# Kernel tuning notes

Measured on AMD Instinct MI355X. Metric: run time of the kernel, lower is better.

The kernel has to match this reference:

```python
import jax, jax.numpy as jnp
import numpy as np

N, E, R, G = 50000, 800000, 8, 128
IN_EMBD, LAYER, OUT = 64, 256, 256
CARDS = [33, 5, 3, 4, 2, 3]
EPS = 1e-5


def setup_inputs() -> dict:
    key = jax.random.key(0)
    ks = iter(jax.random.split(key, 40))
    d = {}
    # int inputs
    cols = [jax.random.randint(next(ks), (N,), 0, c) for c in CARDS]
    d['x'] = jnp.stack(cols, axis=1)                                  # [N,6]
    d['edge_index'] = jax.random.randint(next(ks), (2, E), 0, N)      # [2,E]
    d['edge_type'] = jax.random.randint(next(ks), (E,), 0, R)         # [E]
    d['batch'] = jnp.sort(jax.random.randint(next(ks), (N,), 0, G))   # [N]
    # embedding tables
    for i, c in enumerate(CARDS):
        d[f'emb{i}'] = jax.random.normal(next(ks), (c, IN_EMBD), jnp.float32)
    # RGCNConv1
    d['W1'] = jax.random.normal(next(ks), (R, 6 * IN_EMBD, LAYER), jnp.float32) * 0.05
    d['root1'] = jax.random.normal(next(ks), (6 * IN_EMBD, LAYER), jnp.float32) * 0.05
    d['b1'] = jnp.zeros((LAYER,), jnp.float32)
    # RGCNConv2
    d['W2'] = jax.random.normal(next(ks), (R, LAYER, OUT), jnp.float32) * 0.05
    d['root2'] = jax.random.normal(next(ks), (LAYER, OUT), jnp.float32) * 0.05
    d['b2'] = jnp.zeros((OUT,), jnp.float32)
    # gate_nn: Linear -> BatchNorm1d -> ReLU -> Linear(.,1)
    d['Wg1'] = jax.random.normal(next(ks), (OUT, OUT), jnp.float32) * 0.05
    d['bg1'] = jnp.zeros((OUT,), jnp.float32)
    d['gamma'] = jnp.ones((OUT,), jnp.float32)
    d['beta'] = jnp.zeros((OUT,), jnp.float32)
    d['Wg2'] = jax.random.normal(next(ks), (OUT, 1), jnp.float32) * 0.05
    d['bg2'] = jnp.zeros((1,), jnp.float32)
    # graph head
    d['Wgl'] = jax.random.normal(next(ks), (OUT, 1), jnp.float32) * 0.05
    d['bgl'] = jnp.zeros((1,), jnp.float32)
    return d


def rgcn_conv(h, src, dst, etype, W, root, b):
    # per-relation transform of all nodes, then gather per edge (avoids per-edge weight gather)
    hr = jnp.einsum('ni,rio->rno', h, W)            # [R,N,out]
    msg = hr[etype, src]                             # [E,out]
    # mean aggregation per (dst, relation), matching PyG RGCNConv default aggr='mean'
    counts = jnp.zeros((h.shape[0], W.shape[0]), h.dtype).at[dst, etype].add(1.0)
    norm = 1.0 / jnp.clip(counts, 1.0)               # [N,R]
    agg = jax.ops.segment_sum(msg * norm[dst, etype][:, None], dst, num_segments=h.shape[0])
    return agg + h @ root + b


def global_attention(x, batch, Wg1, bg1, gamma, beta, Wg2, bg2):
    h = x @ Wg1 + bg1
    mu = jnp.mean(h, axis=0)
    var = jnp.var(h, axis=0)
    h = (h - mu) * jax.lax.rsqrt(var + EPS) * gamma + beta   # BatchNorm1d (batch stats)
    gate = jax.nn.relu(h) @ Wg2 + bg2                        # [N,1]
    gmax = jax.ops.segment_max(gate, batch, num_segments=G)
    e = jnp.exp(gate - gmax[batch])
    denom = jax.ops.segment_sum(e, batch, num_segments=G)
    alpha = e / denom[batch]
    return jax.ops.segment_sum(alpha * x, batch, num_segments=G)  # [G,out]


def reference(x, edge_index, edge_type, batch,
              emb0, emb1, emb2, emb3, emb4, emb5,
              W1, root1, b1, W2, root2, b2,
              Wg1, bg1, gamma, beta, Wg2, bg2, Wgl, bgl):
    tables = [emb0, emb1, emb2, emb3, emb4, emb5]
    h = jnp.concatenate([tables[i][x[:, i]] for i in range(6)], axis=1)  # [N, 6*in_embd]
    src, dst = edge_index[0], edge_index[1]
    h = jax.nn.sigmoid(rgcn_conv(h, src, dst, edge_type, W1, root1, b1))
    h = jax.nn.sigmoid(rgcn_conv(h, src, dst, edge_type, W2, root2, b2))
    pooled = global_attention(h, batch, Wg1, bg1, gamma, beta, Wg2, bg2)
    return jax.nn.sigmoid(pooled @ Wgl + bgl)  # [G,1]
```

## Files before the change

kernel.cpp:

```cpp
#include <hip/hip_runtime.h>
#include <hip/hip_bf16.h>
#include <cstdint>

#define NN 50000
#define EE 800000
#define RR 8
#define GG 128
#define D0 384
#define DL 256
#define NCR 50

typedef __attribute__((ext_vector_type(8))) short bf16x8;
typedef __attribute__((ext_vector_type(4))) float f32x4;

__device__ __forceinline__ float sigmoidf_(float x) { return 1.0f / (1.0f + expf(-x)); }

__device__ __forceinline__ ushort f2bf(float f) {
    uint u = __float_as_uint(f);
    u += 0x7fffu + ((u >> 16) & 1u);
    return (ushort)(u >> 16);
}
__device__ __forceinline__ uint pack2bf(float lo, float hi) {
    return (uint)f2bf(lo) | ((uint)f2bf(hi) << 16);
}
__device__ __forceinline__ float bf2f(ushort u) {
    return __uint_as_float((uint)u << 16);
}

__device__ __forceinline__ void accw8(float* s, uint4 a, float w) {
    s[0] += w * __uint_as_float(a.x << 16);
    s[1] += w * __uint_as_float(a.x & 0xffff0000u);
    s[2] += w * __uint_as_float(a.y << 16);
    s[3] += w * __uint_as_float(a.y & 0xffff0000u);
    s[4] += w * __uint_as_float(a.z << 16);
    s[5] += w * __uint_as_float(a.z & 0xffff0000u);
    s[6] += w * __uint_as_float(a.w << 16);
    s[7] += w * __uint_as_float(a.w & 0xffff0000u);
}

__device__ __forceinline__ void unp8(float* f, uint4 a) {
    f[0] = __uint_as_float(a.x << 16);
    f[1] = __uint_as_float(a.x & 0xffff0000u);
    f[2] = __uint_as_float(a.y << 16);
    f[3] = __uint_as_float(a.y & 0xffff0000u);
    f[4] = __uint_as_float(a.z << 16);
    f[5] = __uint_as_float(a.z & 0xffff0000u);
    f[6] = __uint_as_float(a.w << 16);
    f[7] = __uint_as_float(a.w & 0xffff0000u);
}
__device__ __forceinline__ uint4 pack8bf(const float* f) {
    uint4 p;
    p.x = pack2bf(f[0], f[1]);
    p.y = pack2bf(f[2], f[3]);
    p.z = pack2bf(f[4], f[5]);
    p.w = pack2bf(f[6], f[7]);
    return p;
}

__device__ __forceinline__ unsigned fenc(float x) {
    unsigned u = __float_as_uint(x);
    return (u & 0x80000000u) ? ~u : (u | 0x80000000u);
}
__device__ __forceinline__ float fdec(unsigned u) {
    unsigned b = (u & 0x80000000u) ? (u & 0x7fffffffu) : ~u;
    return __uint_as_float(b);
}

__global__ __launch_bounds__(256) void lutbuild_kernel(
    const float* __restrict__ e0, const float* __restrict__ e1,
    const float* __restrict__ e2, const float* __restrict__ e3,
    const float* __restrict__ e4, const float* __restrict__ e5,
    const float* __restrict__ W1, const float* __restrict__ root1,
    ushort* __restrict__ T)
{
    int b = blockIdx.x;
    int cr = b / 9;
    int r  = b - cr * 9;
    int t, c;
    if      (cr < 33) { t = 0; c = cr; }
    else if (cr < 38) { t = 1; c = cr - 33; }
    else if (cr < 41) { t = 2; c = cr - 38; }
    else if (cr < 45) { t = 3; c = cr - 41; }
    else if (cr < 47) { t = 4; c = cr - 45; }
    else              { t = 5; c = cr - 47; }
    const float* emb;
    switch (t) {
        case 0: emb = e0; break; case 1: emb = e1; break; case 2: emb = e2; break;
        case 3: emb = e3; break; case 4: emb = e4; break; default: emb = e5; break;
    }
    const float* er = emb + c * 64;
    int col = threadIdx.x;
    const float* Wb = (r < 8) ? (W1 + ((size_t)r * D0 + t * 64) * DL + col)
                              : (root1 + (size_t)(t * 64) * DL + col);
    float s = 0.f;
    #pragma unroll 8
    for (int k = 0; k < 64; k++) s += er[k] * Wb[(size_t)k * DL];
    T[(size_t)(cr * 9 + r) * DL + col] = f2bf(s);
}

__global__ __launch_bounds__(256) void lutsum_kernel(
    const ushort* __restrict__ T,
    const int* __restrict__ x,
    ushort* __restrict__ hrc,
    int c0, int chc)
{
    __shared__ ushort Ts[NCR * 256];
    const int rr = blockIdx.y;
    int t = threadIdx.x;
    for (int i = t; i < NCR * 256; i += 256) {
        int cr = i >> 8, col = i & 255;
        Ts[i] = T[(size_t)(cr * 9 + c0 + rr) * 256 + col];
    }
    __syncthreads();

    const int slot = t >> 5;
    const int l    = t & 31;
    const int c    = l * 8;
    const int colbase = rr * 256 + c;

    for (int base = blockIdx.x * 8; base < NN; base += gridDim.x * 8) {
        int n = base + slot;
        if (n < NN) {
            const int* xp = x + n * 6;
            const int cumc[6] = {0, 33, 38, 41, 45, 47};
            float acc[8];
            #pragma unroll
            for (int q = 0; q < 8; q++) acc[q] = 0.f;
            #pragma unroll
            for (int tb = 0; tb < 6; tb++) {
                int cr = cumc[tb] + xp[tb];
                uint4 v = *(const uint4*)&Ts[cr * 256 + c];
                accw8(acc, v, 1.0f);
            }
            *(uint4*)&hrc[(size_t)n * chc + colbase] = pack8bf(acc);
        }
    }
}

__global__ __launch_bounds__(256) void lutfin_kernel(
    const ushort* __restrict__ T, const int* __restrict__ x,
    const ushort* __restrict__ hacc, const float* __restrict__ b1,
    ushort* __restrict__ h1)
{
    __shared__ ushort Ts[NCR * 256];
    int t = threadIdx.x;
    for (int i = t; i < NCR * 256; i += 256) {
        int cr = i >> 8, col = i & 255;
        Ts[i] = T[(size_t)(cr * 9 + 8) * 256 + col];
    }
    __syncthreads();

    const int slot = t >> 5;
    const int l = t & 31;
    const int c = l * 8;

    for (int base = blockIdx.x * 8; base < NN; base += gridDim.x * 8) {
        int n = base + slot;
        if (n < NN) {
            const int* xp = x + n * 6;
            const int cumc[6] = {0, 33, 38, 41, 45, 47};
            float acc[8];
            float4 b0 = *(const float4*)&b1[c];
            float4 bb = *(const float4*)&b1[c + 4];
            acc[0] = b0.x; acc[1] = b0.y; acc[2] = b0.z; acc[3] = b0.w;
            acc[4] = bb.x; acc[5] = bb.y; acc[6] = bb.z; acc[7] = bb.w;
            #pragma unroll
            for (int tb = 0; tb < 6; tb++) {
                int cr = cumc[tb] + xp[tb];
                uint4 v = *(const uint4*)&Ts[cr * 256 + c];
                accw8(acc, v, 1.0f);
            }
            uint4 hv = *(const uint4*)&hacc[(size_t)n * DL + c];
            float hf[8]; unp8(hf, hv);
            #pragma unroll
            for (int q = 0; q < 8; q++) acc[q] = sigmoidf_(acc[q] + hf[q]);
            *(uint4*)&h1[(size_t)n * DL + c] = pack8bf(acc);
        }
    }
}

__global__ __launch_bounds__(256) void cvtT_kernel(
    const float* __restrict__ W, const float* __restrict__ root,
    ushort* __restrict__ WbT, int nrel, int IN)
{
    int idx = blockIdx.x * 256 + threadIdx.x;
    int tot = (nrel + 1) * DL * IN;
    if (idx >= tot) return;
    int k = idx % IN;
    int rn = idx / IN;
    int n = rn % DL;
    int r = rn / DL;
    float v = (r < nrel) ? W[((size_t)r * IN + k) * DL + n] : root[(size_t)k * DL + n];
    WbT[idx] = f2bf(v);
}

__global__ __launch_bounds__(256) void count_kernel(
    const int* __restrict__ dst, const int* __restrict__ et, int* __restrict__ counts)
{
    int i = blockIdx.x * 256 + threadIdx.x;
    if (i < EE) atomicAdd(&counts[dst[i] * RR + et[i]], 1);
}

#define SCAN_CHUNK 4096
__global__ __launch_bounds__(256) void scanA_kernel(const int* __restrict__ cnt, int M, int* __restrict__ blkSums)
{
    __shared__ int s[256];
    int b = blockIdx.x, t = threadIdx.x;
    int base = b * SCAN_CHUNK + t * 16;
    int tot = 0;
    #pragma unroll
    for (int i = 0; i < 16; i++) { int idx = base + i; if (idx < M) tot += cnt[idx]; }
    s[t] = tot; __syncthreads();
    for (int off = 128; off > 0; off >>= 1) {
        if (t < off) s[t] += s[t + off];
        __syncthreads();
    }
    if (t == 0) blkSums[b] = s[0];
}

__global__ void scanB_kernel(const int* __restrict__ blkSums, int NB, int* __restrict__ blkOff)
{
    int l = threadIdx.x;
    int a = (l < NB) ? blkSums[l] : 0;
    int b = (64 + l < NB) ? blkSums[64 + l] : 0;
    int ia = a, ib = b;
    for (int o = 1; o < 64; o <<= 1) {
        int t0 = __shfl_up(ia, o, 64);
        if (l >= o) ia += t0;
        int t1 = __shfl_up(ib, o, 64);
        if (l >= o) ib += t1;
    }
    int tot0 = __shfl(ia, 63, 64);
    if (l < NB) blkOff[l] = ia - a;
    if (64 + l < NB) blkOff[64 + l] = tot0 + ib - b;
}

__global__ __launch_bounds__(256) void scanC_kernel(
    const int* __restrict__ cnt, int M, const int* __restrict__ blkOff,
    int* __restrict__ offs, int* __restrict__ curs)
{
    __shared__ int s[256];
    int b = blockIdx.x, t = threadIdx.x;
    int base = b * SCAN_CHUNK + t * 16;
    int loc[16];
    int tot = 0;
    #pragma unroll
    for (int i = 0; i < 16; i++) {
        int idx = base + i;
        int v = (idx < M) ? cnt[idx] : 0;
        loc[i] = tot; tot += v;
    }
    s[t] = tot; __syncthreads();
    for (int off = 1; off < 256; off <<= 1) {
        int v = (t >= off) ? s[t - off] : 0;
        __syncthreads();
        s[t] += v;
        __syncthreads();
    }
    int texc = s[t] - tot;
    int bb = blkOff[b];
    #pragma unroll
    for (int i = 0; i < 16; i++) {
        int idx = base + i;
        if (idx < M) { int o = bb + texc + loc[i]; offs[idx] = o; curs[idx] = o; }
    }
}

__global__ __launch_bounds__(256) void scatter_kernel(
    const int* __restrict__ src, const int* __restrict__ dst, const int* __restrict__ et,
    const int* __restrict__ cnts, int* __restrict__ cursors,
    int2* __restrict__ epk, int chc, int mask)
{
    int i = blockIdx.x * 256 + threadIdx.x;
    if (i < EE) {
        int r = et[i];
        int b = dst[i] * RR + r;
        int pos = atomicAdd(&cursors[b], 1);
        int2 p;
        p.x = src[i] * chc + (r & mask) * DL;
        p.y = __float_as_int(1.0f / (float)cnts[b]);
        epk[pos] = p;
    }
}

template<int K, int MODE>
__global__ __launch_bounds__(256) void dense_gemm(
    const ushort* __restrict__ A,
    const ushort* __restrict__ Bt,
    const float* __restrict__ bias,
    const ushort* __restrict__ haccp,
    ushort* __restrict__ C,
    int M, int NCOL)
{
    constexpr int NKT = K / 64;
    __shared__ __attribute__((aligned(16))) ushort Al[2][128 * 64];
    __shared__ __attribute__((aligned(16))) ushort Bl[2][128 * 64];

    const int nwg  = gridDim.x * gridDim.y;
    const int flat = blockIdx.y * gridDim.x + blockIdx.x;
    const int q8 = nwg >> 3, r8 = nwg & 7;
    const int xcd = flat & 7, pos = flat >> 3;
    const int vid = ((xcd < r8) ? xcd * (q8 + 1) : r8 * (q8 + 1) + (xcd - r8) * q8) + pos;
    const int m0  = (vid / gridDim.x) * 128;
    const int n0  = (vid % gridDim.x) * 128;

    const int t    = threadIdx.x;
    const int lane = t & 63;
    const int wv   = t >> 6;
    const int wr   = (wv >> 1) * 64;
    const int wc   = (wv & 1) * 64;
    const int l15  = lane & 15;
    const int kg   = lane >> 4;

    const int sr = t >> 3;
    const int sc = (t & 7) * 8;
    const int g0 = sc,      g1 = sc + 4;
    const int s0 = ((g0 >> 5) << 2) + ((g0 & 15) >> 2), h0_ = (g0 >> 4) & 1;
    const int s1 = ((g1 >> 5) << 2) + ((g1 & 15) >> 2), h1_ = (g1 >> 4) & 1;

    int arow[4], brow[4];
    #pragma unroll
    for (int i = 0; i < 4; i++) {
        int r = sr + i * 32;
        arow[i] = min(m0 + r, M - 1);
        brow[i] = n0 + r;
    }

    uint4 av[4], bv[4];
    auto SLOAD = [&](int kt) {
        const ushort* Ak = A + kt * 64 + sc;
        const ushort* Bk = Bt + kt * 64 + sc;
        #pragma unroll
        for (int i = 0; i < 4; i++) av[i] = *(const uint4*)(Ak + (size_t)arow[i] * K);
        #pragma unroll
        for (int i = 0; i < 4; i++) bv[i] = *(const uint4*)(Bk + (size_t)brow[i] * K);
    };
    auto SWRITE = [&](int buf) {
        #pragma unroll
        for (int i = 0; i < 4; i++) {
            int row = sr + i * 32;
            int rx  = row & 7;
            int o0  = row * 64 + (((s0 ^ rx) << 3) + h0_ * 4);
            int o1  = row * 64 + (((s1 ^ rx) << 3) + h1_ * 4);
            *(uint2*)&Al[buf][o0] = make_uint2(av[i].x, av[i].y);
            *(uint2*)&Al[buf][o1] = make_uint2(av[i].z, av[i].w);
            *(uint2*)&Bl[buf][o0] = make_uint2(bv[i].x, bv[i].y);
            *(uint2*)&Bl[buf][o1] = make_uint2(bv[i].z, bv[i].w);
        }
    };

    f32x4 acc[4][4];
    #pragma unroll
    for (int mt = 0; mt < 4; mt++)
        #pragma unroll
        for (int nt = 0; nt < 4; nt++) acc[mt][nt] = (f32x4){0.f, 0.f, 0.f, 0.f};

    union FR { bf16x8 v; uint u[4]; };

    SLOAD(0);
    SWRITE(0);
    __syncthreads();

    for (int kt = 0; kt < NKT; kt++) {
        const int cur = kt & 1;
        if (kt + 1 < NKT) {
            SLOAD(kt + 1);
            __builtin_amdgcn_sched_barrier(0);
        }
        const ushort* Ap = Al[cur];
        const ushort* Bp = Bl[cur];
        #pragma unroll
        for (int kb = 0; kb < 2; kb++) {
            const int s = kb * 4 + kg;
            FR a[4], b[4];
            #pragma unroll
            for (int mt = 0; mt < 4; mt++) {
                int row = wr + mt * 16 + l15;
                uint4 va = *(const uint4*)&Ap[row * 64 + ((s ^ (row & 7)) << 3)];
                a[mt].u[0] = va.x; a[mt].u[1] = va.y; a[mt].u[2] = va.z; a[mt].u[3] = va.w;
            }
            #pragma unroll
            for (int nt = 0; nt < 4; nt++) {
                int row = wc + nt * 16 + l15;
                uint4 vb = *(const uint4*)&Bp[row * 64 + ((s ^ (row & 7)) << 3)];
                b[nt].u[0] = vb.x; b[nt].u[1] = vb.y; b[nt].u[2] = vb.z; b[nt].u[3] = vb.w;
            }
            #pragma unroll
            for (int nt = 0; nt < 4; nt++)
                #pragma unroll
                for (int mt = 0; mt < 4; mt++)
                    acc[mt][nt] = __builtin_amdgcn_mfma_f32_16x16x32_bf16(a[mt].v, b[nt].v, acc[mt][nt], 0, 0, 0);
        }
        if (kt + 1 < NKT) {
            SWRITE(cur ^ 1);
            __syncthreads();
        }
    }

    #pragma unroll
    for (int nt = 0; nt < 4; nt++) {
        int col = n0 + wc + nt * 16 + l15;
        float bvv = (MODE >= 1) ? bias[col] : 0.f;
        #pragma unroll
        for (int mt = 0; mt < 4; mt++) {
            #pragma unroll
            for (int i = 0; i < 4; i++) {
                int row = m0 + wr + mt * 16 + kg * 4 + i;
                if (row < M) {
                    float v = acc[mt][nt][i] + bvv;
                    if (MODE == 2) {
                        v += bf2f(haccp[(size_t)row * DL + col]);
                        v = sigmoidf_(v);
                    }
                    C[(size_t)row * NCOL + col] = f2bf(v);
                }
            }
        }
    }
}

__global__ __launch_bounds__(256) void gather_acc(
    const ushort* __restrict__ hrc,
    const int2* __restrict__ epk,
    const int* __restrict__ offs,
    ushort* __restrict__ hacc,
    int relStart, int relEnd, int first)
{
    int t = threadIdx.x;
    int slot = t >> 5;
    int l = t & 31;
    int n = blockIdx.x * 8 + slot;
    if (n >= NN) return;
    int e    = offs[n * 8 + relStart];
    int endE = (relEnd == 8 && n == NN - 1) ? EE : offs[n * 8 + relEnd];
    int c = l * 8;

    float acc[8];
    if (first) {
        #pragma unroll
        for (int q = 0; q < 8; q++) acc[q] = 0.f;
    } else {
        uint4 a = *(const uint4*)&hacc[(size_t)n * DL + c];
        unp8(acc, a);
    }

    for (; e < endE; e += 4) {
        int e1 = min(e + 1, endE - 1);
        int e2 = min(e + 2, endE - 1);
        int e3 = min(e + 3, endE - 1);
        int2 p0 = epk[e], p1 = epk[e1], p2 = epk[e2], p3 = epk[e3];
        float w0 = __int_as_float(p0.y);
        float w1 = (e + 1 < endE) ? __int_as_float(p1.y) : 0.f;
        float w2 = (e + 2 < endE) ? __int_as_float(p2.y) : 0.f;
        float w3 = (e + 3 < endE) ? __int_as_float(p3.y) : 0.f;
        uint4 v0 = *(const uint4*)&hrc[(size_t)p0.x + c];
        uint4 v1 = *(const uint4*)&hrc[(size_t)p1.x + c];
        uint4 v2 = *(const uint4*)&hrc[(size_t)p2.x + c];
        uint4 v3 = *(const uint4*)&hrc[(size_t)p3.x + c];
        accw8(acc, v0, w0); accw8(acc, v1, w1);
        accw8(acc, v2, w2); accw8(acc, v3, w3);
    }

    *(uint4*)&hacc[(size_t)n * DL + c] = pack8bf(acc);
}

__global__ __launch_bounds__(256) void bnstats_kernel(
    const ushort* __restrict__ hg1, float* __restrict__ colsum, float* __restrict__ colsum2)
{
    __shared__ float ss[8][256], ss2[8][256];
    int t = threadIdx.x;
    int g = t >> 5, l = t & 31;
    int c = l * 8;
    constexpr int RPB = (NN + 255) / 256;
    int row0 = blockIdx.x * RPB;
    int rend = min(row0 + RPB, NN);
    float s[8], s2[8];
    #pragma unroll
    for (int q = 0; q < 8; q++) { s[q] = 0.f; s2[q] = 0.f; }
    for (int r = row0 + g; r < rend; r += 8) {
        uint4 v = *(const uint4*)&hg1[(size_t)r * DL + c];
        float f[8]; unp8(f, v);
        #pragma unroll
        for (int q = 0; q < 8; q++) { s[q] += f[q]; s2[q] += f[q] * f[q]; }
    }
    #pragma unroll
    for (int q = 0; q < 8; q++) { ss[g][c + q] = s[q]; ss2[g][c + q] = s2[q]; }
    __syncthreads();
    float ts = 0.f, ts2 = 0.f;
    #pragma unroll
    for (int gg = 0; gg < 8; gg++) { ts += ss[gg][t]; ts2 += ss2[gg][t]; }
    atomicAdd(&colsum[t], ts);
    atomicAdd(&colsum2[t], ts2);
}

__global__ void bnfinal_kernel(
    const float* __restrict__ colsum, const float* __restrict__ colsum2,
    const float* __restrict__ gamma, float* __restrict__ mu, float* __restrict__ aa)
{
    int c = threadIdx.x;
    if (c < DL) {
        float m = colsum[c] / (float)NN;
        float var = colsum2[c] / (float)NN - m * m;
        mu[c] = m;
        aa[c] = rsqrtf(var + 1e-5f) * gamma[c];
    }
}

__global__ __launch_bounds__(256) void gate_kernel(
    const ushort* __restrict__ hg1, const float* __restrict__ mu,
    const float* __restrict__ aa, const float* __restrict__ beta,
    const float* __restrict__ Wg2, const float* __restrict__ bg2,
    const int* __restrict__ batch,
    float* __restrict__ gate, unsigned* __restrict__ gmaxu)
{
    int lane = threadIdx.x & 63;
    int wid = (blockIdx.x * blockDim.x + threadIdx.x) >> 6;
    int nw = (gridDim.x * blockDim.x) >> 6;
    int per = (NN + nw - 1) / nw;
    int n0 = wid * per;
    if (n0 >= NN) return;
    int n1 = min(n0 + per, NN);
    float bg2v = bg2[0];
    float lmax = -3.4e38f;
    int curb = batch[n0];
    for (int n = n0; n < n1; n++) {
        float s = 0.f;
        #pragma unroll
        for (int c = 0; c < 4; c++) {
            int d = c * 64 + lane;
            float v = bf2f(hg1[(size_t)n * DL + d]);
            float xn = (v - mu[d]) * aa[d] + beta[d];
            xn = fmaxf(xn, 0.f);
            s += xn * Wg2[d];
        }
        #pragma unroll
        for (int o = 32; o > 0; o >>= 1) s += __shfl_down(s, o, 64);
        if (lane == 0) {
            float g = s + bg2v;
            gate[n] = g;
            int b = batch[n];
            if (b != curb) {
                atomicMax(&gmaxu[curb], fenc(lmax));
                lmax = -3.4e38f; curb = b;
            }
            lmax = fmaxf(lmax, g);
        }
    }
    if (lane == 0) atomicMax(&gmaxu[curb], fenc(lmax));
}

__global__ __launch_bounds__(256) void expdenom_kernel(
    const float* __restrict__ gate, const int* __restrict__ batch,
    const unsigned* __restrict__ gmaxu, float* __restrict__ ealpha, float* __restrict__ denom)
{
    int tid = blockIdx.x * 256 + threadIdx.x;
    int i0 = tid * 4;
    if (i0 >= NN) return;
    int i1 = min(i0 + 4, NN);
    int curb = batch[i0];
    float m = fdec(gmaxu[curb]);
    float lsum = 0.f;
    for (int i = i0; i < i1; i++) {
        int b = batch[i];
        if (b != curb) {
            atomicAdd(&denom[curb], lsum);
            lsum = 0.f; curb = b; m = fdec(gmaxu[b]);
        }
        float ex = expf(gate[i] - m);
        ealpha[i] = ex;
        lsum += ex;
    }
    atomicAdd(&denom[curb], lsum);
}

__global__ __launch_bounds__(256) void pool_kernel(
    const ushort* __restrict__ h2, const float* __restrict__ ealpha,
    const float* __restrict__ denom, const int* __restrict__ batch,
    float* __restrict__ pooled)
{
    int t = threadIdx.x;
    int g = t >> 5, l = t & 31;
    int c = l * 8;
    int row0 = blockIdx.x * 128 + g * 16;
    if (row0 >= NN) return;
    int rend = min(row0 + 16, NN);
    float acc[8];
    #pragma unroll
    for (int q = 0; q < 8; q++) acc[q] = 0.f;
    int curg = batch[row0];
    for (int r = row0; r < rend; r++) {
        int gb = batch[r];
        if (gb != curg) {
            float inv = 1.0f / denom[curg];
            #pragma unroll
            for (int q = 0; q < 8; q++) atomicAdd(&pooled[curg * DL + c + q], acc[q] * inv);
            #pragma unroll
            for (int q = 0; q < 8; q++) acc[q] = 0.f;
            curg = gb;
        }
        float w = ealpha[r];
        uint4 v = *(const uint4*)&h2[(size_t)r * DL + c];
        accw8(acc, v, w);
    }
    float inv = 1.0f / denom[curg];
    #pragma unroll
    for (int q = 0; q < 8; q++) atomicAdd(&pooled[curg * DL + c + q], acc[q] * inv);
}

__global__ void head_kernel(
    const float* __restrict__ pooled, const float* __restrict__ Wgl,
    const float* __restrict__ bgl, float* __restrict__ out)
{
    int g = blockIdx.x;
    int lane = threadIdx.x;
    float s = 0.f;
    #pragma unroll
    for (int c = 0; c < 4; c++) {
        int d = c * 64 + lane;
        s += pooled[g * DL + d] * Wgl[d];
    }
    #pragma unroll
    for (int o = 32; o > 0; o >>= 1) s += __shfl_down(s, o, 64);
    if (lane == 0) out[g] = sigmoidf_(s + bgl[0]);
}

extern "C" void kernel_launch(void* const* d_in, const int* in_sizes, int n_in,
                              void* d_out, int out_size, void* d_ws, size_t ws_size,
                              hipStream_t stream)
{
    const int* x      = (const int*)d_in[0];
    const int* ei     = (const int*)d_in[1];
    const int* etype  = (const int*)d_in[2];
    const int* batch  = (const int*)d_in[3];
    const float* e0   = (const float*)d_in[4];
    const float* e1   = (const float*)d_in[5];
    const float* e2   = (const float*)d_in[6];
    const float* e3   = (const float*)d_in[7];
    const float* e4   = (const float*)d_in[8];
    const float* e5   = (const float*)d_in[9];
    const float* W1   = (const float*)d_in[10];
    const float* root1= (const float*)d_in[11];
    const float* b1   = (const float*)d_in[12];
    const float* W2   = (const float*)d_in[13];
    const float* root2= (const float*)d_in[14];
    const float* b2   = (const float*)d_in[15];
    const float* Wg1  = (const float*)d_in[16];
    const float* bg1  = (const float*)d_in[17];
    const float* gamma= (const float*)d_in[18];
    const float* beta = (const float*)d_in[19];
    const float* Wg2  = (const float*)d_in[20];
    const float* bg2  = (const float*)d_in[21];
    const float* Wgl  = (const float*)d_in[22];
    const float* bgl  = (const float*)d_in[23];
    float* out = (float*)d_out;

    const int* esrc_in = ei;
    const int* edst_in = ei + EE;

    char* ws = (char*)d_ws;
    size_t off = 0;
    auto alloc = [&](size_t b) -> char* {
        char* p = ws + off;
        off += (b + 255) & ~(size_t)255;
        return p;
    };
    ushort* h2     = (ushort*)alloc((size_t)NN * DL * 2);
    ushort* h1     = (ushort*)alloc((size_t)NN * DL * 2);
    ushort* hacc   = (ushort*)alloc((size_t)NN * DL * 2);
    size_t zstart = off;
    int*      counts  = (int*)alloc((size_t)NN * RR * 4);
    float*    colsum  = (float*)alloc(DL * 4);
    float*    colsum2 = (float*)alloc(DL * 4);
    unsigned* gmaxu   = (unsigned*)alloc(GG * 4);
    float*    denom   = (float*)alloc(GG * 4);
    float*    pooled  = (float*)alloc((size_t)GG * DL * 4);
    size_t zbytes = off - zstart;
    int*   offs    = (int*)alloc((size_t)NN * RR * 4);
    int*   cursors = (int*)alloc((size_t)NN * RR * 4);
    int2*  epk     = (int2*)alloc((size_t)EE * 8);
    int*   blkSums = (int*)alloc(512);
    int*   blkOff  = (int*)alloc(512);
    float* mu      = (float*)alloc(DL * 4);
    float* aa      = (float*)alloc(DL * 4);
    float* gate    = (float*)alloc((size_t)NN * 4);
    float* ealpha  = (float*)alloc((size_t)NN * 4);
    ushort* Tlut   = (ushort*)alloc((size_t)NCR * 9 * DL * 2);
    ushort* WbT2   = (ushort*)alloc((size_t)9 * DL * DL * 2);
    ushort* WbTg   = (ushort*)alloc((size_t)1 * DL * DL * 2);

    int npc;
    ushort* hrc;
    {
        size_t need4 = ((size_t)NN * 4 * DL * 2 + 255) & ~(size_t)255;
        size_t need2 = ((size_t)NN * 2 * DL * 2 + 255) & ~(size_t)255;
        if (off + need4 <= ws_size)      { npc = 4; hrc = (ushort*)alloc((size_t)NN * 4 * DL * 2); }
        else if (off + need2 <= ws_size) { npc = 2; hrc = (ushort*)alloc((size_t)NN * 2 * DL * 2); }
        else return;
    }
    const int chc = npc * DL;

    ushort* hg1 = hrc;

    hipMemsetAsync(ws + zstart, 0, zbytes, stream);

    lutbuild_kernel<<<NCR * 9, 256, 0, stream>>>(e0, e1, e2, e3, e4, e5, W1, root1, Tlut);
    count_kernel<<<(EE + 255) / 256, 256, 0, stream>>>(edst_in, etype, counts);
    {
        int tot2 = 9 * DL * DL;
        cvtT_kernel<<<(tot2 + 255) / 256, 256, 0, stream>>>(W2, root2, WbT2, RR, DL);
        int totg = 1 * DL * DL;
        cvtT_kernel<<<(totg + 255) / 256, 256, 0, stream>>>(nullptr, Wg1, WbTg, 0, DL);
    }

    const int M = NN * RR;
    const int NB = (M + SCAN_CHUNK - 1) / SCAN_CHUNK;
    scanA_kernel<<<NB, 256, 0, stream>>>(counts, M, blkSums);
    scanB_kernel<<<1, 64, 0, stream>>>(blkSums, NB, blkOff);
    scanC_kernel<<<NB, 256, 0, stream>>>(counts, M, blkOff, offs, cursors);
    scatter_kernel<<<(EE + 255) / 256, 256, 0, stream>>>(esrc_in, edst_in, etype, counts, cursors,
                                                          epk, chc, npc - 1);

    const int MT = (NN + 127) / 128;
    const dim3 GC(npc * 2, MT), G2(2, MT);
    const int ABLK = (NN + 7) / 8;

    for (int c0 = 0; c0 < RR; c0 += npc) {
        dim3 LG(512, npc);
        lutsum_kernel<<<LG, 256, 0, stream>>>(Tlut, x, hrc, c0, chc);
        gather_acc<<<ABLK, 256, 0, stream>>>(hrc, epk, offs, hacc, c0, c0 + npc, c0 == 0);
    }
    lutfin_kernel<<<512, 256, 0, stream>>>(Tlut, x, hacc, b1, h1);

    for (int c0 = 0; c0 < RR; c0 += npc) {
        dense_gemm<DL, 0><<<GC, 256, 0, stream>>>(h1, WbT2 + (size_t)c0 * DL * DL, nullptr, nullptr, hrc, NN, chc);
        gather_acc<<<ABLK, 256, 0, stream>>>(hrc, epk, offs, hacc, c0, c0 + npc, c0 == 0);
    }
    dense_gemm<DL, 2><<<G2, 256, 0, stream>>>(h1, WbT2 + (size_t)8 * DL * DL, b2, hacc, h2, NN, DL);

    dense_gemm<DL, 1><<<G2, 256, 0, stream>>>(h2, WbTg, bg1, nullptr, hg1, NN, DL);

    bnstats_kernel<<<256, 256, 0, stream>>>(hg1, colsum, colsum2);
    bnfinal_kernel<<<1, 256, 0, stream>>>(colsum, colsum2, gamma, mu, aa);
    gate_kernel<<<512, 256, 0, stream>>>(hg1, mu, aa, beta, Wg2, bg2, batch, gate, gmaxu);
    expdenom_kernel<<<((NN + 3) / 4 + 255) / 256, 256, 0, stream>>>(gate, batch, gmaxu, ealpha, denom);
    pool_kernel<<<(NN + 127) / 128, 256, 0, stream>>>(h2, ealpha, denom, batch, pooled);
    head_kernel<<<GG, 64, 0, stream>>>(pooled, Wgl, bgl, out);
}
```

Baseline: 623.4 us.

## Fuse layer-1 LUT sum into edge gather, skipping per-relation node transform buffer

Layer 1 previously materialized a per-relation transformed node buffer (LUT sums written to hrc) and then gathered it per edge. Now a fused gather_lut kernel loads the per-relation LUT slices into shared memory. For each incoming edge it recomputes the source node's transformed row from its six categorical indices, so the large intermediate write and read are gone. Edge records now pack src*8+r, and gather_acc decodes them. The trade is six LDS reads per edge instead of one global read, plus extra reads of x for every edge.

Result: slower. 638.5 us (+2.4%).

```diff
diff --git a/kernel.cpp b/kernel.cpp
--- a/kernel.cpp
+++ b/kernel.cpp
@@ -98,43 +98,73 @@
     T[(size_t)(cr * 9 + r) * DL + col] = f2bf(s);
 }
 
-__global__ __launch_bounds__(256) void lutsum_kernel(
+__global__ __launch_bounds__(256) void gather_lut(
     const ushort* __restrict__ T,
     const int* __restrict__ x,
-    ushort* __restrict__ hrc,
-    int c0, int chc)
-{
-    __shared__ ushort Ts[NCR * 256];
-    const int rr = blockIdx.y;
+    const int2* __restrict__ epk,
+    const int* __restrict__ offs,
+    ushort* __restrict__ hacc,
+    int r0, int first)
+{
+    constexpr int STR = 72;
+    __shared__ ushort Ts[4 * NCR * STR];
+    const int q = blockIdx.y;
     int t = threadIdx.x;
-    for (int i = t; i < NCR * 256; i += 256) {
-        int cr = i >> 8, col = i & 255;
-        Ts[i] = T[(size_t)(cr * 9 + c0 + rr) * 256 + col];
+    for (int i = t; i < 4 * NCR * 8; i += 256) {
+        int row = i >> 3, j = i & 7;
+        int r = row / NCR, cr = row - r * NCR;
+        uint4 v = *(const uint4*)&T[(size_t)(cr * 9 + r0 + r) * 256 + q * 64 + j * 8];
+        *(uint4*)&Ts[row * STR + j * 8] = v;
     }
     __syncthreads();
 
-    const int slot = t >> 5;
-    const int l    = t & 31;
+    const int slot = t >> 3;
+    const int l    = t & 7;
     const int c    = l * 8;
-    const int colbase = rr * 256 + c;
-
-    for (int base = blockIdx.x * 8; base < NN; base += gridDim.x * 8) {
-        int n = base + slot;
-        if (n < NN) {
-            const int* xp = x + n * 6;
-            const int cumc[6] = {0, 33, 38, 41, 45, 47};
-            float acc[8];
-            #pragma unroll
-            for (int q = 0; q < 8; q++) acc[q] = 0.f;
-            #pragma unroll
-            for (int tb = 0; tb < 6; tb++) {
-                int cr = cumc[tb] + xp[tb];
-                uint4 v = *(const uint4*)&Ts[cr * 256 + c];
-                accw8(acc, v, 1.0f);
-            }
-            *(uint4*)&hrc[(size_t)n * chc + colbase] = pack8bf(acc);
-        }
-    }
+
+    int n = blockIdx.x * 32 + slot;
+    if (n >= NN) return;
+    int e    = offs[n * 8 + r0];
+    int endE = (r0 + 4 == 8) ? ((n == NN - 1) ? EE : offs[n * 8 + 8])
+                             : offs[n * 8 + r0 + 4];
+
+    float acc[8];
+    if (first) {
+        #pragma unroll
+        for (int qq = 0; qq < 8; qq++) acc[qq] = 0.f;
+    } else {
+        uint4 a = *(const uint4*)&hacc[(size_t)n * DL + q * 64 + c];
+        unp8(acc, a);
+    }
+
+    const int cumc[6] = {0, 33, 38, 41, 45, 47};
+    for (; e < endE; e += 2) {
+        int e1 = min(e + 1, endE - 1);
+        int2 p0 = epk[e], p1 = epk[e1];
+        float w0 = __int_as_float(p0.y);
+        float w1 = (e + 1 < endE) ? __int_as_float(p1.y) : 0.f;
+        int s0 = p0.x >> 3, ra = (p0.x & 7) - r0;
+        int s1 = p1.x >> 3, rb = (p1.x & 7) - r0;
+        const int* xp0 = x + s0 * 6;
+        const int* xp1 = x + s1 * 6;
+        int cra[6], crb[6];
+        #pragma unroll
+        for (int tb = 0; tb < 6; tb++) { cra[tb] = cumc[tb] + xp0[tb]; }
+        #pragma unroll
+        for (int tb = 0; tb < 6; tb++) { crb[tb] = cumc[tb] + xp1[tb]; }
+        #pragma unroll
+        for (int tb = 0; tb < 6; tb++) {
+            uint4 v = *(const uint4*)&Ts[(ra * NCR + cra[tb]) * STR + c];
+            accw8(acc, v, w0);
+        }
+        #pragma unroll
+        for (int tb = 0; tb < 6; tb++) {
+            uint4 v = *(const uint4*)&Ts[(rb * NCR + crb[tb]) * STR + c];
+            accw8(acc, v, w1);
+        }
+    }
+
+    *(uint4*)&hacc[(size_t)n * DL + q * 64 + c] = pack8bf(acc);
 }
 
 __global__ __launch_bounds__(256) void lutfin_kernel(
@@ -269,7 +299,7 @@
 __global__ __launch_bounds__(256) void scatter_kernel(
     const int* __restrict__ src, const int* __restrict__ dst, const int* __restrict__ et,
     const int* __restrict__ cnts, int* __restrict__ cursors,
-    int2* __restrict__ epk, int chc, int mask)
+    int2* __restrict__ epk)
 {
     int i = blockIdx.x * 256 + threadIdx.x;
     if (i < EE) {
@@ -277,7 +307,7 @@
         int b = dst[i] * RR + r;
         int pos = atomicAdd(&cursors[b], 1);
         int2 p;
-        p.x = src[i] * chc + (r & mask) * DL;
+        p.x = src[i] * 8 + r;
         p.y = __float_as_int(1.0f / (float)cnts[b]);
         epk[pos] = p;
     }
@@ -424,7 +454,7 @@
     const int2* __restrict__ epk,
     const int* __restrict__ offs,
     ushort* __restrict__ hacc,
-    int relStart, int relEnd, int first)
+    int relStart, int relEnd, int first, int chc, int mask)
 {
     int t = threadIdx.x;
     int slot = t >> 5;
@@ -453,10 +483,14 @@
         float w1 = (e + 1 < endE) ? __int_as_float(p1.y) : 0.f;
         float w2 = (e + 2 < endE) ? __int_as_float(p2.y) : 0.f;
         float w3 = (e + 3 < endE) ? __int_as_float(p3.y) : 0.f;
-        uint4 v0 = *(const uint4*)&hrc[(size_t)p0.x + c];
-        uint4 v1 = *(const uint4*)&hrc[(size_t)p1.x + c];
-        uint4 v2 = *(const uint4*)&hrc[(size_t)p2.x + c];
-        uint4 v3 = *(const uint4*)&hrc[(size_t)p3.x + c];
+        int i0 = (p0.x >> 3) * chc + ((p0.x & 7) & mask) * DL;
+        int i1 = (p1.x >> 3) * chc + ((p1.x & 7) & mask) * DL;
+        int i2 = (p2.x >> 3) * chc + ((p2.x & 7) & mask) * DL;
+        int i3 = (p3.x >> 3) * chc + ((p3.x & 7) & mask) * DL;
+        uint4 v0 = *(const uint4*)&hrc[(size_t)i0 + c];
+        uint4 v1 = *(const uint4*)&hrc[(size_t)i1 + c];
+        uint4 v2 = *(const uint4*)&hrc[(size_t)i2 + c];
+        uint4 v3 = *(const uint4*)&hrc[(size_t)i3 + c];
         accw8(acc, v0, w0); accw8(acc, v1, w1);
         accw8(acc, v2, w2); accw8(acc, v3, w3);
     }
@@ -717,23 +751,22 @@
     scanA_kernel<<<NB, 256, 0, stream>>>(counts, M, blkSums);
     scanB_kernel<<<1, 64, 0, stream>>>(blkSums, NB, blkOff);
     scanC_kernel<<<NB, 256, 0, stream>>>(counts, M, blkOff, offs, cursors);
-    scatter_kernel<<<(EE + 255) / 256, 256, 0, stream>>>(esrc_in, edst_in, etype, counts, cursors,
-                                                          epk, chc, npc - 1);
+    scatter_kernel<<<(EE + 255) / 256, 256, 0, stream>>>(esrc_in, edst_in, etype, counts, cursors, epk);
 
     const int MT = (NN + 127) / 128;
     const dim3 GC(npc * 2, MT), G2(2, MT);
     const int ABLK = (NN + 7) / 8;
 
-    for (int c0 = 0; c0 < RR; c0 += npc) {
-        dim3 LG(512, npc);
-        lutsum_kernel<<<LG, 256, 0, stream>>>(Tlut, x, hrc, c0, chc);
-        gather_acc<<<ABLK, 256, 0, stream>>>(hrc, epk, offs, hacc, c0, c0 + npc, c0 == 0);
+    {
+        dim3 GL((NN + 31) / 32, 4);
+        gather_lut<<<GL, 256, 0, stream>>>(Tlut, x, epk, offs, hacc, 0, 1);
+        gather_lut<<<GL, 256, 0, stream>>>(Tlut, x, epk, offs, hacc, 4, 0);
     }
     lutfin_kernel<<<512, 256, 0, stream>>>(Tlut, x, hacc, b1, h1);
 
     for (int c0 = 0; c0 < RR; c0 += npc) {
         dense_gemm<DL, 0><<<GC, 256, 0, stream>>>(h1, WbT2 + (size_t)c0 * DL * DL, nullptr, nullptr, hrc, NN, chc);
-        gather_acc<<<ABLK, 256, 0, stream>>>(hrc, epk, offs, hacc, c0, c0 + npc, c0 == 0);
+        gather_acc<<<ABLK, 256, 0, stream>>>(hrc, epk, offs, hacc, c0, c0 + npc, c0 == 0, chc, npc - 1);
     }
     dense_gemm<DL, 2><<<G2, 256, 0, stream>>>(h1, WbT2 + (size_t)8 * DL * DL, b2, hacc, h2, NN, DL);
 
```
